# Optimization experiments

Measured on AMD Instinct MI355X. Metric: run time of the kernel, lower is better.

## Reference

```python
import jax, jax.numpy as jnp
import numpy as np

NUM_GRAPHS = 1024
SLOPE = 0.01  # LeakyReLU default negative slope

def lrelu(v):
    return jnp.where(v >= 0, v, SLOPE * v)

def setup_inputs() -> dict:
    key = jax.random.key(0)
    ks = jax.random.split(key, 16)
    N, D, H, K = 131072, 128, 512, 256
    s = 0.02
    inp = {
        "x": jax.random.normal(ks[0], (N, D), dtype=jnp.float32),
        "batch_ids": jnp.sort(jax.random.randint(ks[1], (N,), 0, NUM_GRAPHS, dtype=jnp.int32)),
        "ge_W0": s * jax.random.normal(ks[2], (D, H), dtype=jnp.float32),
        "ge_b0": jnp.zeros((H,), jnp.float32),
        "ge_Wh": s * jax.random.normal(ks[3], (2, H, H), dtype=jnp.float32),
        "ge_bh": jnp.zeros((2, H), jnp.float32),
        "ge_Wo": s * jax.random.normal(ks[4], (H, K), dtype=jnp.float32),
        "ge_bo": jnp.zeros((K,), jnp.float32),
        "in_W": s * jax.random.normal(ks[5], (D, H), dtype=jnp.float32),
        "in_b": jnp.zeros((H,), jnp.float32),
        "ag_W": s * jax.random.normal(ks[6], (K, H), dtype=jnp.float32),
        "ag_b": jnp.zeros((H,), jnp.float32),
        "psi_Wh": s * jax.random.normal(ks[7], (3, H, H), dtype=jnp.float32),
        "psi_bh": jnp.zeros((3, H), jnp.float32),
        "psi_Wo": s * jax.random.normal(ks[8], (H, D), dtype=jnp.float32),
        "psi_bo": jnp.zeros((D,), jnp.float32),
    }
    return inp

def reference(x, batch_ids, ge_W0, ge_b0, ge_Wh, ge_bh, ge_Wo, ge_bo,
              in_W, in_b, ag_W, ag_b, psi_Wh, psi_bh, psi_Wo, psi_bo):
    # --- GlobalEmbedding: phi MLP (LeakyReLU between layers, none after last) ---
    h = lrelu(x @ ge_W0 + ge_b0)                     # [N, H]
    for i in range(ge_Wh.shape[0]):                  # fixed n_layers-1 hidden linears
        h = lrelu(h @ ge_Wh[i] + ge_bh[i])
    h = h @ ge_Wo + ge_bo                            # [N, K]
    node_emb = lrelu(h)                              # trailing activation in GlobalEmbedding
    # mean aggregation per graph (ptr-based segment mean)
    sums = jax.ops.segment_sum(node_emb, batch_ids, num_segments=NUM_GRAPHS)  # [G, K]
    counts = jax.ops.segment_sum(jnp.ones((x.shape[0],), x.dtype), batch_ids, num_segments=NUM_GRAPHS)
    sigma = sums / jnp.maximum(counts, 1.0)[:, None]                          # [G, K]
    # --- broadcast-gather + fused residual MLP ---
    sigma_hid = sigma @ ag_W + ag_b                  # [G, H]
    x_hid = x @ in_W + in_b                          # [N, H]
    p = lrelu(x_hid + sigma_hid[batch_ids])          # gather per node, [N, H]
    for i in range(psi_Wh.shape[0]):
        p = lrelu(p @ psi_Wh[i] + psi_bh[i])
    out = p @ psi_Wo + psi_bo                        # [N, D]
    return out
```

## Files before the change

kernel.cpp:

```cpp
#include <hip/hip_runtime.h>
#include <hip/hip_bf16.h>


typedef __attribute__((ext_vector_type(8))) short bf16x8;
typedef __attribute__((ext_vector_type(4))) float f32x4;

#define N_NODES 131072
#define NUM_G   1024

__device__ __forceinline__ float lrelu_f(float v) { return v >= 0.f ? v : 0.01f * v; }
__device__ __forceinline__ short f2bs(float f) {
  union { __hip_bfloat16 h; short s; } q; q.h = __float2bfloat16(f); return q.s;
}
__device__ __forceinline__ float bs2f(unsigned short u) {
  unsigned x = ((unsigned)u) << 16; return __uint_as_float(x);
}
__device__ __forceinline__ void gll16(const __hip_bfloat16* g, char* l) {
  __builtin_amdgcn_global_load_lds((const __attribute__((address_space(1))) void*)g,
                                   (__attribute__((address_space(3))) void*)l, 16, 0, 0);
}

__global__ void sentinel(float* out, float v) {
  if (blockIdx.x == 0 && threadIdx.x == 0) out[0] = v;
}

__global__ void wt_conv(const float* __restrict__ W, __hip_bfloat16* __restrict__ WT, int K, int P) {
  __shared__ float tile[32][33];
  const int p0 = blockIdx.x << 5, k0 = blockIdx.y << 5;
  const int tx = threadIdx.x & 31, ty = threadIdx.x >> 5;
#pragma unroll
  for (int i = 0; i < 4; ++i) {
    int r = ty + (i << 3);
    tile[r][tx] = W[(size_t)(k0 + r) * P + p0 + tx];
  }
  __syncthreads();
#pragma unroll
  for (int i = 0; i < 4; ++i) {
    int r = ty + (i << 3);
    WT[(size_t)(p0 + r) * K + k0 + tx] = __float2bfloat16(tile[tx][r]);
  }
}

template<int SHIFT>
__global__ void wt_convC(const float* __restrict__ W, __hip_bfloat16* __restrict__ WTc) {
  int idx = blockIdx.x * 256 + threadIdx.x;
  int p = idx & ((1 << SHIFT) - 1);
  int k = idx >> SHIFT;
  WTc[((size_t)((k >> 3) << SHIFT) + p) * 8 + (k & 7)] = __float2bfloat16(W[idx]);
}

__global__ void sigma_fin(const float* __restrict__ sums,
                          const int* __restrict__ ids,
                          __hip_bfloat16* __restrict__ sigma) {
  int g = blockIdx.x;
  int k = threadIdx.x;
  int lo = 0, hi = N_NODES;
  while (lo < hi) { int m = (lo + hi) >> 1; if (ids[m] < g) lo = m + 1; else hi = m; }
  int s = lo;
  hi = N_NODES;
  while (lo < hi) { int m = (lo + hi) >> 1; if (ids[m] < g + 1) lo = m + 1; else hi = m; }
  int e = lo;
  float c = (float)(e - s);
  sigma[g * 256 + k] = __float2bfloat16(sums[g * 256 + k] / fmaxf(c, 1.f));
}

template<int ACT, int BF16OUT>
__global__ __launch_bounds__(256)
void gemm_mfma(const __hip_bfloat16* __restrict__ A,
               const __hip_bfloat16* __restrict__ BT,
               const float* __restrict__ bias,
               void* __restrict__ out, int K, int P) {
  __shared__ __attribute__((aligned(128))) char smem[81920];
  const int tid  = threadIdx.x;
  const int lane = tid & 63;
  const int wave = tid >> 6;
  const int bcol = blockIdx.x << 7;
  const int brow = blockIdx.y << 7;
  const int wm = (wave >> 1) << 6;
  const int wn = (wave & 1) << 6;
  const int lrow = lane >> 2;
  const int gc   = (lane & 3) ^ ((lane >> 3) & 3);
  f32x4 acc[4][4] = {};
  const int nt = K >> 5;
  auto STAGE = [&](int t) {
    char* sA = smem + (t % 5) * 16384;
    char* sB = sA + 8192;
    const int k0 = t << 5;
#pragma unroll
    for (int i = 0; i < 2; ++i) {
      int seg = (wave << 1) + i;
      int row = (seg << 4) + lrow;
      gll16(A + (size_t)(brow + row) * K + (k0 + (gc << 3)), sA + (seg << 10));
      gll16(BT + (size_t)(bcol + row) * K + (k0 + (gc << 3)), sB + (seg << 10));
    }
  };
  STAGE(0); STAGE(1); STAGE(2);
  const int r15 = lane & 15;
  const int c   = lane >> 4;
  for (int t = 0; t < nt; ++t) {
    if (t + 3 < nt) STAGE(t + 3);
    const int rem = nt - 1 - t;
    if (rem >= 3)      asm volatile("s_waitcnt vmcnt(12)" ::: "memory");
    else if (rem == 2) asm volatile("s_waitcnt vmcnt(8)"  ::: "memory");
    else if (rem == 1) asm volatile("s_waitcnt vmcnt(4)"  ::: "memory");
    else               asm volatile("s_waitcnt vmcnt(0)"  ::: "memory");
    __builtin_amdgcn_s_barrier();
    __builtin_amdgcn_sched_barrier(0);
    char* sA = smem + (t % 5) * 16384;
    char* sB = sA + 8192;
    bf16x8 af[4], bfv[4];
#pragma unroll
    for (int f = 0; f < 4; ++f) {
      int ar = wm + (f << 4) + r15;
      af[f]  = *reinterpret_cast<const bf16x8*>(sA + ar * 64 + ((c ^ ((ar >> 1) & 3)) << 4));
      int br = wn + (f << 4) + r15;
      bfv[f] = *reinterpret_cast<const bf16x8*>(sB + br * 64 + ((c ^ ((br >> 1) & 3)) << 4));
    }
#pragma unroll
    for (int fm = 0; fm < 4; ++fm)
#pragma unroll
      for (int fn = 0; fn < 4; ++fn)
        acc[fm][fn] = __builtin_amdgcn_mfma_f32_16x16x32_bf16(af[fm], bfv[fn], acc[fm][fn], 0, 0, 0);
  }
  const int hi4 = (lane >> 4) << 2;
#pragma unroll
  for (int fn = 0; fn < 4; ++fn) {
    int col = bcol + wn + (fn << 4) + r15;
    float bv = bias[col];
#pragma unroll
    for (int fm = 0; fm < 4; ++fm) {
      int row0 = brow + wm + (fm << 4) + hi4;
#pragma unroll
      for (int r = 0; r < 4; ++r) {
        float v = acc[fm][fn][r] + bv;
        if (ACT) v = lrelu_f(v);
        size_t oidx = (size_t)(row0 + r) * P + col;
        if (BF16OUT) reinterpret_cast<__hip_bfloat16*>(out)[oidx] = __float2bfloat16(v);
        else         reinterpret_cast<float*>(out)[oidx] = v;
      }
    }
  }
}

template<int K, int P, int MODE>
__device__ __forceinline__ void layer8(
    char* actmem, const __hip_bfloat16* __restrict__ WTs,
    const float* __restrict__ bias, const float* __restrict__ sh,
    const int* __restrict__ ids, float* __restrict__ gout, int nbase, int tid) {
  const int w = tid >> 6, lane = tid & 63;
  const int r15 = lane & 15, khi = lane >> 4;
  constexpr int PW = P >> 3;
  constexpr int MF = PW >> 4;
  constexpr int NT = K >> 5;
  const int p0w = w * PW;
  const bf16x8* __restrict__ WTg = reinterpret_cast<const bf16x8*>(WTs);
  const size_t gb = (size_t)khi * P + p0w + r15;

  f32x4 acc[MF][4];
#pragma unroll
  for (int a = 0; a < MF; ++a)
#pragma unroll
    for (int b = 0; b < 4; ++b) acc[a][b] = f32x4{0.f, 0.f, 0.f, 0.f};

#pragma unroll
  for (int t = 0; t < NT; ++t) {
    bf16x8 af[MF], bf[4];
#pragma unroll
    for (int mi = 0; mi < MF; ++mi)
      af[mi] = WTg[gb + (size_t)(t << 2) * P + (mi << 4)];
    const int chsw = ((t << 2) + khi) ^ (r15 & 7);
#pragma unroll
    for (int ni = 0; ni < 4; ++ni) {
      int nd = (ni << 4) + r15;
      bf[ni] = *reinterpret_cast<const bf16x8*>(actmem + (nd << 10) + (chsw << 4));
    }
#pragma unroll
    for (int mi = 0; mi < MF; ++mi)
#pragma unroll
      for (int ni = 0; ni < 4; ++ni)
        acc[mi][ni] = __builtin_amdgcn_mfma_f32_16x16x32_bf16(af[mi], bf[ni], acc[mi][ni], 0, 0, 0);
  }

  if constexpr (MODE == 3) {
    const int pb = p0w + (khi << 2);
    f32x4 bv = *reinterpret_cast<const f32x4*>(bias + pb);
#pragma unroll
    for (int ni = 0; ni < 4; ++ni) {
      int nd = (ni << 4) + r15;
      f32x4 v = acc[0][ni] + bv;
      *reinterpret_cast<f32x4*>(gout + ((size_t)(nbase + nd) << 7) + pb) = v;
    }
  } else {
    __syncthreads();
#pragma unroll
    for (int mi = 0; mi < MF; ++mi) {
      const int pb = p0w + (mi << 4) + (khi << 2);
      f32x4 bv = *reinterpret_cast<const f32x4*>(bias + pb);
#pragma unroll
      for (int ni = 0; ni < 4; ++ni) {
        int nd = (ni << 4) + r15;
        f32x4 v = acc[mi][ni] + bv;
        if constexpr (MODE == 1) {
          int g = ids[nbase + nd];
          f32x4 s = *reinterpret_cast<const f32x4*>(sh + ((size_t)g << 9) + pb);
          v = v + s;
        }
        short4 u;
        u.x = f2bs(lrelu_f(v[0])); u.y = f2bs(lrelu_f(v[1]));
        u.z = f2bs(lrelu_f(v[2])); u.w = f2bs(lrelu_f(v[3]));
        int ch = (pb >> 3) ^ (nd & 7);
        *reinterpret_cast<short4*>(actmem + (nd << 10) + (ch << 4) + ((pb & 4) << 1)) = u;
      }
    }
    __syncthreads();

    if constexpr (MODE == 2) {
      const int c = tid & 255, h = tid >> 8;
      float a = 0.f;
      int gp = ids[nbase + (h << 5)];
      for (int r = 0; r < 32; ++r) {
        int nd = (h << 5) + r;
        int ch = (c >> 3) ^ (nd & 7);
        unsigned short uv = *reinterpret_cast<const unsigned short*>(
            actmem + (nd << 10) + (ch << 4) + ((c & 7) << 1));
        float v = bs2f(uv);
        int g = ids[nbase + nd];
        if (g != gp) { atomicAdd(gout + ((size_t)gp << 8) + c, a); a = 0.f; gp = g; }
        a += v;
      }
      atomicAdd(gout + ((size_t)gp << 8) + c, a);
    }
  }
}

template<int PSI>
__global__ __launch_bounds__(512, 1)
void fused_chain8(const float* __restrict__ x, const int* __restrict__ bids,
                  const __hip_bfloat16* __restrict__ Wa, const float* __restrict__ ba,
                  const __hip_bfloat16* __restrict__ Wb, const float* __restrict__ bb,
                  const __hip_bfloat16* __restrict__ Wc, const float* __restrict__ bc,
                  const __hip_bfloat16* __restrict__ Wd, const float* __restrict__ bd,
                  const __hip_bfloat16* __restrict__ We, const float* __restrict__ be,
                  const float* __restrict__ sh, float* __restrict__ gout) {
  __shared__ __attribute__((aligned(128))) char actmem[65536];
  const int tid = threadIdx.x;
  const int nbase = blockIdx.x << 6;

#pragma unroll
  for (int i = 0; i < 2; ++i) {
    int L = (i << 9) + tid;
    int n = L >> 4, c = L & 15;
    const float* xp = x + (((size_t)(nbase + n)) << 7) + (c << 3);
    float4 v0 = *reinterpret_cast<const float4*>(xp);
    float4 v1 = *reinterpret_cast<const float4*>(xp + 4);
    bf16x8 pk;
    pk[0] = f2bs(v0.x); pk[1] = f2bs(v0.y); pk[2] = f2bs(v0.z); pk[3] = f2bs(v0.w);
    pk[4] = f2bs(v1.x); pk[5] = f2bs(v1.y); pk[6] = f2bs(v1.z); pk[7] = f2bs(v1.w);
    *reinterpret_cast<bf16x8*>(actmem + (n << 10) + ((c ^ (n & 7)) << 4)) = pk;
  }
  __syncthreads();

  if constexpr (PSI == 0) {
    layer8<128, 512, 0>(actmem, Wa, ba, nullptr, bids, nullptr, nbase, tid);
    layer8<512, 512, 0>(actmem, Wb, bb, nullptr, bids, nullptr, nbase, tid);
    layer8<512, 512, 0>(actmem, Wc, bc, nullptr, bids, nullptr, nbase, tid);
    layer8<512, 256, 2>(actmem, Wd, bd, nullptr, bids, gout, nbase, tid);
  } else {
    layer8<128, 512, 1>(actmem, Wa, ba, sh, bids, nullptr, nbase, tid);
    layer8<512, 512, 0>(actmem, Wb, bb, nullptr, bids, nullptr, nbase, tid);
    layer8<512, 512, 0>(actmem, Wc, bc, nullptr, bids, nullptr, nbase, tid);
    layer8<512, 512, 0>(actmem, Wd, bd, nullptr, bids, nullptr, nbase, tid);
    layer8<512, 128, 3>(actmem, We, be, nullptr, bids, gout, nbase, tid);
  }
}

extern "C" void kernel_launch(void* const* d_in, const int* in_sizes, int n_in,
                              void* d_out, int out_size, void* d_ws, size_t ws_size,
                              hipStream_t stream) {
  const float* x      = (const float*)d_in[0];
  const int*   bids   = (const int*)  d_in[1];
  const float* ge_W0  = (const float*)d_in[2];
  const float* ge_b0  = (const float*)d_in[3];
  const float* ge_Wh  = (const float*)d_in[4];
  const float* ge_bh  = (const float*)d_in[5];
  const float* ge_Wo  = (const float*)d_in[6];
  const float* ge_bo  = (const float*)d_in[7];
  const float* in_W   = (const float*)d_in[8];
  const float* in_b   = (const float*)d_in[9];
  const float* ag_W   = (const float*)d_in[10];
  const float* ag_b   = (const float*)d_in[11];
  const float* psi_Wh = (const float*)d_in[12];
  const float* psi_bh = (const float*)d_in[13];
  const float* psi_Wo = (const float*)d_in[14];
  const float* psi_bo = (const float*)d_in[15];

  char* ws = (char*)d_ws;
  __hip_bfloat16* geW0C   = (__hip_bfloat16*)(ws + 0);
  __hip_bfloat16* geWh0C  = (__hip_bfloat16*)(ws + 131072);
  __hip_bfloat16* geWh1C  = (__hip_bfloat16*)(ws + 655360);
  __hip_bfloat16* geWoC   = (__hip_bfloat16*)(ws + 1179648);
  __hip_bfloat16* inWC    = (__hip_bfloat16*)(ws + 1441792);
  __hip_bfloat16* agWT    = (__hip_bfloat16*)(ws + 1572864);
  __hip_bfloat16* psiWh0C = (__hip_bfloat16*)(ws + 1835008);
  __hip_bfloat16* psiWh1C = (__hip_bfloat16*)(ws + 2359296);
  __hip_bfloat16* psiWh2C = (__hip_bfloat16*)(ws + 2883584);
  __hip_bfloat16* psiWoC  = (__hip_bfloat16*)(ws + 3407872);
  __hip_bfloat16* sigma   = (__hip_bfloat16*)(ws + 3538944);
  float*          sh      = (float*)         (ws + 4063232);
  float*          sums    = (float*)         (ws + 6160384);

  if (ws_size < 7340032) {
    sentinel<<<1, 64, 0, stream>>>((float*)d_out, 100000000.f + (float)(ws_size / 1024));
    return;
  }

  dim3 blk(256);
  hipMemsetAsync(sums, 0, NUM_G * 256 * sizeof(float), stream);

  wt_convC<9><<<256,  blk, 0, stream>>>(ge_W0,           geW0C);
  wt_convC<9><<<1024, blk, 0, stream>>>(ge_Wh,           geWh0C);
  wt_convC<9><<<1024, blk, 0, stream>>>(ge_Wh + 262144,  geWh1C);
  wt_convC<8><<<512,  blk, 0, stream>>>(ge_Wo,           geWoC);
  wt_convC<9><<<256,  blk, 0, stream>>>(in_W,            inWC);
  wt_conv<<<dim3(16, 8), blk, 0, stream>>>(ag_W, agWT, 256, 512);
  wt_convC<9><<<1024, blk, 0, stream>>>(psi_Wh,          psiWh0C);
  wt_convC<9><<<1024, blk, 0, stream>>>(psi_Wh + 262144, psiWh1C);
  wt_convC<9><<<1024, blk, 0, stream>>>(psi_Wh + 524288, psiWh2C);
  wt_convC<7><<<256,  blk, 0, stream>>>(psi_Wo,          psiWoC);

  fused_chain8<0><<<N_NODES / 64, 512, 0, stream>>>(
      x, bids, geW0C, ge_b0, geWh0C, ge_bh, geWh1C, ge_bh + 512, geWoC, ge_bo,
      nullptr, nullptr, nullptr, sums);

  sigma_fin<<<NUM_G, blk, 0, stream>>>(sums, bids, sigma);
  gemm_mfma<0, 0><<<dim3(4, 8), blk, 0, stream>>>(sigma, agWT, ag_b, sh, 256, 512);

  fused_chain8<1><<<N_NODES / 64, 512, 0, stream>>>(
      x, bids, inWC, in_b, psiWh0C, psi_bh, psiWh1C, psi_bh + 512,
      psiWh2C, psi_bh + 1024, psiWoC, psi_bo, sh, (float*)d_out);
}
```

Before: 501.0 us.

## Double node tile to 128 per block, prefetch weight fragments, raise MFMA priority

Each block of the fused MLP chain kernels now handles 128 nodes instead of 64, so every weight fragment loaded from global memory feeds twice as many MFMAs. Activation LDS grows to 128 KB, and each wave holds twice the accumulators. Weight fragments for the next K-step are double-buffered in registers, and the MFMA section runs at raised wave priority. The risks are higher register pressure (possible spills) and half as many blocks (1024), which leaves less parallelism to spread across the CUs.

```diff
diff --git a/kernel.cpp b/kernel.cpp
--- a/kernel.cpp
+++ b/kernel.cpp
@@ -143,7 +143,7 @@
 }
 
 template<int K, int P, int MODE>
-__device__ __forceinline__ void layer8(
+__device__ __forceinline__ void layer13(
     char* actmem, const __hip_bfloat16* __restrict__ WTs,
     const float* __restrict__ bias, const float* __restrict__ sh,
     const int* __restrict__ ids, float* __restrict__ gout, int nbase, int tid) {
@@ -156,36 +156,47 @@
   const bf16x8* __restrict__ WTg = reinterpret_cast<const bf16x8*>(WTs);
   const size_t gb = (size_t)khi * P + p0w + r15;
 
-  f32x4 acc[MF][4];
+  f32x4 acc[MF][8];
 #pragma unroll
   for (int a = 0; a < MF; ++a)
 #pragma unroll
-    for (int b = 0; b < 4; ++b) acc[a][b] = f32x4{0.f, 0.f, 0.f, 0.f};
+    for (int b = 0; b < 8; ++b) acc[a][b] = f32x4{0.f, 0.f, 0.f, 0.f};
+
+  bf16x8 afA[MF], afB[MF];
+#pragma unroll
+  for (int mi = 0; mi < MF; ++mi)
+    afA[mi] = WTg[gb + (mi << 4)];
 
 #pragma unroll
   for (int t = 0; t < NT; ++t) {
-    bf16x8 af[MF], bf[4];
-#pragma unroll
-    for (int mi = 0; mi < MF; ++mi)
-      af[mi] = WTg[gb + (size_t)(t << 2) * P + (mi << 4)];
+    bf16x8* cur = (t & 1) ? afB : afA;
+    bf16x8* nxt = (t & 1) ? afA : afB;
+    if (t + 1 < NT) {
+#pragma unroll
+      for (int mi = 0; mi < MF; ++mi)
+        nxt[mi] = WTg[gb + (size_t)((t + 1) << 2) * P + (mi << 4)];
+    }
+    bf16x8 bf[8];
     const int chsw = ((t << 2) + khi) ^ (r15 & 7);
 #pragma unroll
-    for (int ni = 0; ni < 4; ++ni) {
+    for (int ni = 0; ni < 8; ++ni) {
       int nd = (ni << 4) + r15;
       bf[ni] = *reinterpret_cast<const bf16x8*>(actmem + (nd << 10) + (chsw << 4));
     }
+    __builtin_amdgcn_s_setprio(1);
 #pragma unroll
     for (int mi = 0; mi < MF; ++mi)
 #pragma unroll
-      for (int ni = 0; ni < 4; ++ni)
-        acc[mi][ni] = __builtin_amdgcn_mfma_f32_16x16x32_bf16(af[mi], bf[ni], acc[mi][ni], 0, 0, 0);
+      for (int ni = 0; ni < 8; ++ni)
+        acc[mi][ni] = __builtin_amdgcn_mfma_f32_16x16x32_bf16(cur[mi], bf[ni], acc[mi][ni], 0, 0, 0);
+    __builtin_amdgcn_s_setprio(0);
   }
 
   if constexpr (MODE == 3) {
     const int pb = p0w + (khi << 2);
     f32x4 bv = *reinterpret_cast<const f32x4*>(bias + pb);
 #pragma unroll
-    for (int ni = 0; ni < 4; ++ni) {
+    for (int ni = 0; ni < 8; ++ni) {
       int nd = (ni << 4) + r15;
       f32x4 v = acc[0][ni] + bv;
       *reinterpret_cast<f32x4*>(gout + ((size_t)(nbase + nd) << 7) + pb) = v;
@@ -197,7 +208,7 @@
       const int pb = p0w + (mi << 4) + (khi << 2);
       f32x4 bv = *reinterpret_cast<const f32x4*>(bias + pb);
 #pragma unroll
-      for (int ni = 0; ni < 4; ++ni) {
+      for (int ni = 0; ni < 8; ++ni) {
         int nd = (ni << 4) + r15;
         f32x4 v = acc[mi][ni] + bv;
         if constexpr (MODE == 1) {
@@ -217,9 +228,9 @@
     if constexpr (MODE == 2) {
       const int c = tid & 255, h = tid >> 8;
       float a = 0.f;
-      int gp = ids[nbase + (h << 5)];
-      for (int r = 0; r < 32; ++r) {
-        int nd = (h << 5) + r;
+      int gp = ids[nbase + (h << 6)];
+      for (int r = 0; r < 64; ++r) {
+        int nd = (h << 6) + r;
         int ch = (c >> 3) ^ (nd & 7);
         unsigned short uv = *reinterpret_cast<const unsigned short*>(
             actmem + (nd << 10) + (ch << 4) + ((c & 7) << 1));
@@ -235,19 +246,19 @@
 
 template<int PSI>
 __global__ __launch_bounds__(512, 1)
-void fused_chain8(const float* __restrict__ x, const int* __restrict__ bids,
-                  const __hip_bfloat16* __restrict__ Wa, const float* __restrict__ ba,
-                  const __hip_bfloat16* __restrict__ Wb, const float* __restrict__ bb,
-                  const __hip_bfloat16* __restrict__ Wc, const float* __restrict__ bc,
-                  const __hip_bfloat16* __restrict__ Wd, const float* __restrict__ bd,
-                  const __hip_bfloat16* __restrict__ We, const float* __restrict__ be,
-                  const float* __restrict__ sh, float* __restrict__ gout) {
-  __shared__ __attribute__((aligned(128))) char actmem[65536];
+void fused_chain13(const float* __restrict__ x, const int* __restrict__ bids,
+                   const __hip_bfloat16* __restrict__ Wa, const float* __restrict__ ba,
+                   const __hip_bfloat16* __restrict__ Wb, const float* __restrict__ bb,
+                   const __hip_bfloat16* __restrict__ Wc, const float* __restrict__ bc,
+                   const __hip_bfloat16* __restrict__ Wd, const float* __restrict__ bd,
+                   const __hip_bfloat16* __restrict__ We, const float* __restrict__ be,
+                   const float* __restrict__ sh, float* __restrict__ gout) {
+  __shared__ __attribute__((aligned(128))) char actmem[131072];
   const int tid = threadIdx.x;
-  const int nbase = blockIdx.x << 6;
-
-#pragma unroll
-  for (int i = 0; i < 2; ++i) {
+  const int nbase = blockIdx.x << 7;
+
+#pragma unroll
+  for (int i = 0; i < 4; ++i) {
     int L = (i << 9) + tid;
     int n = L >> 4, c = L & 15;
     const float* xp = x + (((size_t)(nbase + n)) << 7) + (c << 3);
@@ -261,16 +272,16 @@
   __syncthreads();
 
   if constexpr (PSI == 0) {
-    layer8<128, 512, 0>(actmem, Wa, ba, nullptr, bids, nullptr, nbase, tid);
-    layer8<512, 512, 0>(actmem, Wb, bb, nullptr, bids, nullptr, nbase, tid);
-    layer8<512, 512, 0>(actmem, Wc, bc, nullptr, bids, nullptr, nbase, tid);
-    layer8<512, 256, 2>(actmem, Wd, bd, nullptr, bids, gout, nbase, tid);
+    layer13<128, 512, 0>(actmem, Wa, ba, nullptr, bids, nullptr, nbase, tid);
+    layer13<512, 512, 0>(actmem, Wb, bb, nullptr, bids, nullptr, nbase, tid);
+    layer13<512, 512, 0>(actmem, Wc, bc, nullptr, bids, nullptr, nbase, tid);
+    layer13<512, 256, 2>(actmem, Wd, bd, nullptr, bids, gout, nbase, tid);
   } else {
-    layer8<128, 512, 1>(actmem, Wa, ba, sh, bids, nullptr, nbase, tid);
-    layer8<512, 512, 0>(actmem, Wb, bb, nullptr, bids, nullptr, nbase, tid);
-    layer8<512, 512, 0>(actmem, Wc, bc, nullptr, bids, nullptr, nbase, tid);
-    layer8<512, 512, 0>(actmem, Wd, bd, nullptr, bids, nullptr, nbase, tid);
-    layer8<512, 128, 3>(actmem, We, be, nullptr, bids, gout, nbase, tid);
+    layer13<128, 512, 1>(actmem, Wa, ba, sh, bids, nullptr, nbase, tid);
+    layer13<512, 512, 0>(actmem, Wb, bb, nullptr, bids, nullptr, nbase, tid);
+    layer13<512, 512, 0>(actmem, Wc, bc, nullptr, bids, nullptr, nbase, tid);
+    layer13<512, 512, 0>(actmem, Wd, bd, nullptr, bids, nullptr, nbase, tid);
+    layer13<512, 128, 3>(actmem, We, be, nullptr, bids, gout, nbase, tid);
   }
 }
 
@@ -328,14 +339,14 @@
   wt_convC<9><<<1024, blk, 0, stream>>>(psi_Wh + 524288, psiWh2C);
   wt_convC<7><<<256,  blk, 0, stream>>>(psi_Wo,          psiWoC);
 
-  fused_chain8<0><<<N_NODES / 64, 512, 0, stream>>>(
+  fused_chain13<0><<<N_NODES / 128, 512, 0, stream>>>(
       x, bids, geW0C, ge_b0, geWh0C, ge_bh, geWh1C, ge_bh + 512, geWoC, ge_bo,
       nullptr, nullptr, nullptr, sums);
 
   sigma_fin<<<NUM_G, blk, 0, stream>>>(sums, bids, sigma);
   gemm_mfma<0, 0><<<dim3(4, 8), blk, 0, stream>>>(sigma, agWT, ag_b, sh, 256, 512);
 
-  fused_chain8<1><<<N_NODES / 64, 512, 0, stream>>>(
+  fused_chain13<1><<<N_NODES / 128, 512, 0, stream>>>(
       x, bids, inWC, in_b, psiWh0C, psi_bh, psiWh1C, psi_bh + 512,
       psiWh2C, psi_bh + 1024, psiWoC, psi_bo, sh, (float*)d_out);
 }
```

After: 590.4 us. 1.18x slower.
